# Kernel tuning notes

Hardware: AMD Instinct MI355X
Metric: run time of the kernel (lower is better)

## Reference

```python
import jax, jax.numpy as jnp
import numpy as np

H_MODEL = 1024
N_HEADS = 16
N_KV_HEADS = 4
HEAD_DIM = 64
SLIDING_WINDOW = 512
B, S = 2, 2048
NEG_INF = -1e9


def rotate_half(x):
    half = x.shape[-1] // 2
    return jnp.concatenate([-x[..., half:], x[..., :half]], axis=-1)


def setup_inputs() -> dict:
    key = jax.random.key(0)
    ks = jax.random.split(key, 8)
    hidden_states = jax.random.normal(ks[0], (B, S, H_MODEL), dtype=jnp.float32)
    # RoPE tables (HF style): cos/sin of shape [1, S, head_dim]
    inv_freq = 1.0 / (10000.0 ** (jnp.arange(0, HEAD_DIM, 2, dtype=jnp.float32) / HEAD_DIM))
    pos = jnp.arange(S, dtype=jnp.float32)
    freqs = jnp.einsum('s,d->sd', pos, inv_freq)            # [S, D/2]
    emb = jnp.concatenate([freqs, freqs], axis=-1)          # [S, D]
    cos = jnp.cos(emb)[None]                                # [1, S, D]
    sin = jnp.sin(emb)[None]
    # additive causal + sliding-window mask [1,1,S,S]
    i = jnp.arange(S)[:, None]
    j = jnp.arange(S)[None, :]
    allowed = (j <= i) & (i - j < SLIDING_WINDOW)
    attention_mask = jnp.where(allowed, 0.0, NEG_INF).astype(jnp.float32)[None, None]
    # projection weights (torch Linear stores [out, in]; y = x @ W.T)
    std = 0.02
    Wq = jax.random.normal(ks[1], (N_HEADS * HEAD_DIM, H_MODEL), dtype=jnp.float32) * std
    Wk = jax.random.normal(ks[2], (N_KV_HEADS * HEAD_DIM, H_MODEL), dtype=jnp.float32) * std
    Wv = jax.random.normal(ks[3], (N_KV_HEADS * HEAD_DIM, H_MODEL), dtype=jnp.float32) * std
    Wo = jax.random.normal(ks[4], (H_MODEL, N_HEADS * HEAD_DIM), dtype=jnp.float32) * std
    return {"hidden_states": hidden_states, "cos": cos, "sin": sin,
            "attention_mask": attention_mask, "Wq": Wq, "Wk": Wk, "Wv": Wv, "Wo": Wo}


def reference(hidden_states, cos, sin, attention_mask, Wq, Wk, Wv, Wo):
    b, s, _ = hidden_states.shape
    G = N_HEADS // N_KV_HEADS
    scaling = HEAD_DIM ** -0.5
    # QKV projections -> [B, H, S, D]
    q = jnp.einsum('bsh,oh->bso', hidden_states, Wq).reshape(b, s, N_HEADS, HEAD_DIM).transpose(0, 2, 1, 3)
    k = jnp.einsum('bsh,oh->bso', hidden_states, Wk).reshape(b, s, N_KV_HEADS, HEAD_DIM).transpose(0, 2, 1, 3)
    v = jnp.einsum('bsh,oh->bso', hidden_states, Wv).reshape(b, s, N_KV_HEADS, HEAD_DIM).transpose(0, 2, 1, 3)
    # RoPE (cos/sin broadcast over head dim via unsqueeze(1))
    c = cos[:, None, :, :]
    sn = sin[:, None, :, :]
    q = q * c + rotate_half(q) * sn
    k = k * c + rotate_half(k) * sn
    # GQA eager attention: group query heads over kv heads
    qg = q.reshape(b, N_KV_HEADS, G, s, HEAD_DIM)
    scores = jnp.einsum('bkgqd,bkpd->bkgqp', qg, k) * scaling  # [B,Hkv,G,S,S]
    scores = scores + attention_mask[:, :, None, :, :]
    probs = jax.nn.softmax(scores.astype(jnp.float32), axis=-1).astype(q.dtype)
    out = jnp.einsum('bkgqp,bkpd->bkgqd', probs, v)            # [B,Hkv,G,S,D]
    out = out.reshape(b, N_HEADS, s, HEAD_DIM).transpose(0, 2, 1, 3).reshape(b, s, N_HEADS * HEAD_DIM)
    return jnp.einsum('bso,ho->bsh', out, Wo)
```

## Files before the change

kernel.cpp:

```cpp
#include <hip/hip_runtime.h>
#include <hip/hip_bf16.h>

#define S_LEN 2048
#define NH 16
#define NKV 4
#define HD 64
#define WIN 512
#define BATCH 2

typedef __bf16 bf16_8 __attribute__((ext_vector_type(8)));
typedef float f32x4 __attribute__((ext_vector_type(4)));

__device__ inline bf16_8 cvt8(f32x4 a, f32x4 b) {
    bf16_8 r;
    r[0] = (__bf16)a[0]; r[1] = (__bf16)a[1]; r[2] = (__bf16)a[2]; r[3] = (__bf16)a[3];
    r[4] = (__bf16)b[0]; r[5] = (__bf16)b[1]; r[6] = (__bf16)b[2]; r[7] = (__bf16)b[3];
    return r;
}

typedef __attribute__((address_space(1))) const unsigned int guint;
typedef __attribute__((address_space(3))) unsigned int luint;
__device__ __forceinline__ void gload16(const void* g, void* l) {
    __builtin_amdgcn_global_load_lds((guint*)g, (luint*)l, 16, 0, 0);
}


__global__ __launch_bounds__(256) void cvt_pack(
    const float* __restrict__ hs, const float* __restrict__ Wq,
    const float* __restrict__ Wk, const float* __restrict__ Wv,
    const float* __restrict__ Wo,
    __bf16* __restrict__ hsp, __bf16* __restrict__ Wqp,
    __bf16* __restrict__ Wkp, __bf16* __restrict__ Wvp,
    __bf16* __restrict__ Wop)
{
    int i = blockIdx.x * 256 + threadIdx.x;
    const float* S; __bf16* P;
    if (i < 524288)      { S = hs; P = hsp; }
    else if (i < 655360) { S = Wq; P = Wqp; i -= 524288; }
    else if (i < 688128) { S = Wk; P = Wkp; i -= 655360; }
    else if (i < 720896) { S = Wv; P = Wvp; i -= 688128; }
    else                 { S = Wo; P = Wop; i -= 720896; }
    const int n = i >> 7;
    const int k = (i & 127) << 3;
    const f32x4 a = *(const f32x4*)(S + (size_t)n * 1024 + k);
    const f32x4 b = *(const f32x4*)(S + (size_t)n * 1024 + k + 4);
    const size_t dst = ((size_t)((n >> 4) * 32 + (k >> 5)) << 9)
                     + ((size_t)((n & 15) | (((k >> 3) & 3) << 4)) << 3);
    *(bf16_8*)(P + dst) = cvt8(a, b);
}

__device__ __forceinline__ void gemm64x128(
    const __bf16* __restrict__ Apk,
    const __bf16* __restrict__ Bp,
    int bx, int colb,
    __bf16* __restrict__ smem,
    int tid, f32x4 acc[2][4])
{
    const int wave = tid >> 6;
    const int lane = tid & 63;
    const int wm   = wave & 1;
    const int wn   = wave >> 1;
    const int lofs = lane << 3;
    const f32x4 fzero = {0.f, 0.f, 0.f, 0.f};
#pragma unroll
    for (int i = 0; i < 2; ++i)
#pragma unroll
        for (int nt = 0; nt < 4; ++nt) acc[i][nt] = fzero;

    __bf16* As = smem;
    __bf16* Bs = smem + 8192;

    const __bf16* aSrc  = Apk + ((size_t)(bx * 4 + wave) * 32) * 512 + lofs;
    const __bf16* bSrc0 = Bp + ((size_t)((colb >> 4) + wave * 2) * 32) * 512 + lofs;
    const __bf16* bSrc1 = Bp + ((size_t)((colb >> 4) + wave * 2 + 1) * 32) * 512 + lofs;

#define STAGE(buf, it) do {                                            \
        const int ko = (it) * 2;                                       \
        __bf16* ad = As + (buf) * 4096 + wave * 1024;                  \
        gload16(aSrc + (size_t)ko * 512,       ad);                    \
        gload16(aSrc + (size_t)(ko + 1) * 512, ad + 512);              \
        __bf16* bd = Bs + (buf) * 8192 + wave * 2048;                  \
        gload16(bSrc0 + (size_t)ko * 512,       bd);                   \
        gload16(bSrc0 + (size_t)(ko + 1) * 512, bd + 512);             \
        gload16(bSrc1 + (size_t)ko * 512,       bd + 1024);            \
        gload16(bSrc1 + (size_t)(ko + 1) * 512, bd + 1536);            \
    } while (0)

    STAGE(0, 0);
    __syncthreads();

#pragma unroll 2
    for (int it = 0; it < 16; ++it) {
        const int cur = it & 1;
        if (it < 15) STAGE(cur ^ 1, it + 1);

        const __bf16* Ab = As + cur * 4096;
        const __bf16* Bb = Bs + cur * 8192;
#pragma unroll
        for (int ks = 0; ks < 2; ++ks) {
            bf16_8 af[2], bf[4];
#pragma unroll
            for (int i = 0; i < 2; ++i)
                af[i] = *(const bf16_8*)(Ab + ((wm * 2 + i) * 2 + ks) * 512 + lofs);
#pragma unroll
            for (int nt = 0; nt < 4; ++nt)
                bf[nt] = *(const bf16_8*)(Bb + ((wn * 4 + nt) * 2 + ks) * 512 + lofs);
#pragma unroll
            for (int i = 0; i < 2; ++i)
#pragma unroll
                for (int nt = 0; nt < 4; ++nt)
                    acc[i][nt] = __builtin_amdgcn_mfma_f32_16x16x32_bf16(af[i], bf[nt], acc[i][nt], 0, 0, 0);
        }
        __syncthreads();
    }
#undef STAGE
}

__global__ __launch_bounds__(256) void gemm_qkv(
    const __bf16* __restrict__ Apk,
    const __bf16* __restrict__ Wqp,
    const __bf16* __restrict__ Wkp,
    const __bf16* __restrict__ Wvp,
    __bf16* __restrict__ Qp,
    __bf16* __restrict__ Kf,
    __bf16* __restrict__ Vf,
    const float* __restrict__ cosb,
    const float* __restrict__ sinb)
{
    __shared__ __align__(16) __bf16 smem[24576];

    const int tid  = threadIdx.x;
    const int wave = tid >> 6;
    const int lane = tid & 63;
    const int wm   = wave & 1;
    const int wn   = wave >> 1;
    const int fm   = lane & 15;

    const int bx   = blockIdx.x;
    const int row0 = bx * 64;
    const int by   = blockIdx.y;

    const __bf16* Bp; int colb; int mode;
    if (by < 8)       { Bp = Wqp; colb = by * 128;        mode = 0; }
    else if (by < 10) { Bp = Wkp; colb = (by - 8) * 128;  mode = 1; }
    else              { Bp = Wvp; colb = (by - 10) * 128; mode = 2; }
    const int col0 = colb;

    f32x4 acc[2][4];
    gemm64x128(Apk, Bp, bx, colb, smem, tid, acc);

    const int drow = (lane >> 4) << 2;
    const int cq   = col0 + wn * 64;
    const int bb   = row0 >> 11;
    const int sk0  = row0 & (S_LEN - 1);

    if (mode == 0) {
        const int lp = drow | ((fm >> 3) << 4);
#pragma unroll
        for (int i = 0; i < 2; ++i) {
            const size_t t1 = (size_t)(bx * 4 + wm * 2 + i) * 32 + (cq >> 5);
#pragma unroll
            for (int r = 0; r < 4; ++r) {
                const int row = row0 + wm * 32 + i * 16 + drow + r;
                const int s   = row & (S_LEN - 1);
#pragma unroll
                for (int nt = 0; nt < 2; ++nt) {
                    const int d = nt * 16 + fm;
                    const float c1 = cosb[s * HD + d];
                    const float s1 = sinb[s * HD + d];
                    const float c2 = cosb[s * HD + d + 32];
                    const float s2 = sinb[s * HD + d + 32];
                    const float x1 = acc[i][nt][r];
                    const float x2 = acc[i][nt + 2][r];
                    const size_t o = ((size_t)(lp + r + (nt * 2 << 4)) << 3) + (fm & 7);
                    Qp[(t1 << 9) + o]       = (__bf16)(x1 * c1 - x2 * s1);
                    Qp[((t1 + 1) << 9) + o] = (__bf16)(x2 * c2 + x1 * s2);
                }
            }
        }
    } else if (mode == 1) {
        __bf16* T = smem;
#pragma unroll
        for (int i = 0; i < 2; ++i) {
#pragma unroll
            for (int r = 0; r < 4; ++r) {
                const int kl = wm * 32 + i * 16 + drow + r;
                const int s  = sk0 + kl;
#pragma unroll
                for (int nt = 0; nt < 2; ++nt) {
                    const int d = nt * 16 + fm;
                    const float c1 = cosb[s * HD + d];
                    const float s1 = sinb[s * HD + d];
                    const float c2 = cosb[s * HD + d + 32];
                    const float s2 = sinb[s * HD + d + 32];
                    const float x1 = acc[i][nt][r];
                    const float x2 = acc[i][nt + 2][r];
                    T[kl * 136 + wn * 64 + d]      = (__bf16)(x1 * c1 - x2 * s1);
                    T[kl * 136 + wn * 64 + d + 32] = (__bf16)(x2 * c2 + x1 * s2);
                }
            }
        }
        __syncthreads();
#pragma unroll
        for (int c = 0; c < 4; ++c) {
            const int tile = c * 4 + wave;
            const int hh  = tile >> 3;
            const int kt4 = (tile >> 1) & 3;
            const int dd  = tile & 1;
            const int key = kt4 * 16 + fm;
            const int dl  = dd * 32 + ((lane >> 4) << 3);
            const bf16_8 v = *(const bf16_8*)&T[key * 136 + hh * 64 + dl];
            const int khg = (col0 + hh * 64) >> 6;
            const int ktg = (sk0 >> 4) + kt4;
            *(bf16_8*)&Kf[(size_t)(bb * NKV + khg) * 131072 + (size_t)(ktg * 2 + dd) * 512 + lane * 8] = v;
        }
    } else {
        __bf16* T2 = smem;
#pragma unroll
        for (int i = 0; i < 2; ++i)
#pragma unroll
            for (int r = 0; r < 4; ++r)
#pragma unroll
                for (int nt = 0; nt < 4; ++nt)
                    T2[(wn * 64 + nt * 16 + fm) * 72 + wm * 32 + i * 16 + drow + r] =
                        (__bf16)acc[i][nt][r];
        __syncthreads();
#pragma unroll
        for (int c = 0; c < 4; ++c) {
            const int tile = c * 4 + wave;
            const int hh  = tile >> 3;
            const int dd4 = (tile >> 1) & 3;
            const int ks  = tile & 1;
            const int dl  = dd4 * 16 + fm;
            const int key = ks * 32 + ((lane >> 4) << 3);
            const bf16_8 v = *(const bf16_8*)&T2[(hh * 64 + dl) * 72 + key];
            const int khg = (col0 + hh * 64) >> 6;
            const int kvg = (sk0 >> 5) + ks;
            *(bf16_8*)&Vf[(size_t)(bb * NKV + khg) * 131072 + (size_t)(dd4 * 64 + kvg) * 512 + lane * 8] = v;
        }
    }
}

__global__ __launch_bounds__(256) void gemm_o(
    const __bf16* __restrict__ Apk,
    const __bf16* __restrict__ Bp,
    float* __restrict__ C)
{
    __shared__ __align__(16) __bf16 smem[24576];

    const int tid  = threadIdx.x;
    const int wave = tid >> 6;
    const int lane = tid & 63;
    const int wm   = wave & 1;
    const int wn   = wave >> 1;

    const int bx   = blockIdx.x;
    const int row0 = bx * 64;
    const int colb = blockIdx.y * 128;

    f32x4 acc[2][4];
    gemm64x128(Apk, Bp, bx, colb, smem, tid, acc);

    const int fm = lane & 15;
    const int drow = (lane >> 4) << 2;
#pragma unroll
    for (int i = 0; i < 2; ++i)
#pragma unroll
        for (int r = 0; r < 4; ++r) {
            const int row = row0 + wm * 32 + i * 16 + drow + r;
#pragma unroll
            for (int nt = 0; nt < 4; ++nt)
                C[(size_t)row * 1024 + colb + wn * 64 + nt * 16 + fm] = acc[i][nt][r];
        }
}

__global__ __launch_bounds__(256) void attn_pk(const __bf16* __restrict__ Qp,
                                               const __bf16* __restrict__ Kf,
                                               const __bf16* __restrict__ Vf,
                                               __bf16* __restrict__ Op)
{
    __shared__ __align__(16) __bf16 Ps[4][16][72];

    const int tid  = threadIdx.x;
    const int wave = tid >> 6;
    const int lane = tid & 63;

    const int bid0 = blockIdx.x;
    const int bid  = (bid0 & 7) * 128 + (bid0 >> 3);

    const int qt = bid & (S_LEN / 64 - 1);
    const int h  = (bid >> 5) & (NH - 1);
    const int b  = bid >> 9;
    const int kh = h >> 2;

    const int q0 = qt * 64;
    const int qw = q0 + wave * 16;

    const int fm = lane & 15;

    const size_t qtile = ((size_t)((b * S_LEN + qw) >> 4) * 32 + h * 2) << 9;
    const bf16_8 qf0 = *(const bf16_8*)&Qp[qtile + (lane << 3)];
    const bf16_8 qf1 = *(const bf16_8*)&Qp[qtile + 512 + (lane << 3)];

    const __bf16* Kfb = Kf + (size_t)(b * NKV + kh) * 131072 + lane * 8;
    const __bf16* Vfb = Vf + (size_t)(b * NKV + kh) * 131072 + lane * 8;

    const f32x4 fzero = {0.f, 0.f, 0.f, 0.f};
    f32x4 oacc[4];
    float l[4];
#pragma unroll
    for (int nt = 0; nt < 4; ++nt) oacc[nt] = fzero;
#pragma unroll
    for (int r = 0; r < 4; ++r) l[r] = 0.f;

    const int qbase = qw + ((lane >> 4) << 2);
    const int fj = (lane >> 4) << 3;

    const int lo  = (qw >= WIN) ? ((qw - WIN + 1) & ~63) : 0;
    const int hi  = (qw + 15) & ~63;
    const int nit = ((hi - lo) >> 6) + 1;

    for (int it = 0; it < nit; ++it) {
        const int kb = lo + (it << 6);

        f32x4 sc[4];
        const int ktb = kb >> 4;
#pragma unroll
        for (int t4 = 0; t4 < 4; ++t4) {
            const bf16_8 k0 = *(const bf16_8*)(Kfb + (size_t)((ktb + t4) * 2) * 512);
            const bf16_8 k1 = *(const bf16_8*)(Kfb + (size_t)((ktb + t4) * 2 + 1) * 512);
            f32x4 s = fzero;
            s = __builtin_amdgcn_mfma_f32_16x16x32_bf16(qf0, k0, s, 0, 0, 0);
            s = __builtin_amdgcn_mfma_f32_16x16x32_bf16(qf1, k1, s, 0, 0, 0);
            sc[t4] = s;
        }

#pragma unroll
        for (int t4 = 0; t4 < 4; ++t4) {
            const int ki = kb + t4 * 16 + fm;
#pragma unroll
            for (int r = 0; r < 4; ++r) {
                const int qr = qbase + r;
                const float e = __expf(sc[t4][r] * 0.125f);
                const float p = (ki <= qr && qr - ki < WIN) ? e : 0.f;
                l[r] += p;
                Ps[wave][((lane >> 4) << 2) + r][t4 * 16 + fm] = (__bf16)p;
            }
        }

        const bf16_8 pf0 = *(const bf16_8*)&Ps[wave][fm][fj];
        const bf16_8 pf1 = *(const bf16_8*)&Ps[wave][fm][32 + fj];

        const int kvb = kb >> 5;
#pragma unroll
        for (int nt = 0; nt < 4; ++nt) {
            const bf16_8 v0 = *(const bf16_8*)(Vfb + (size_t)(nt * 64 + kvb) * 512);
            const bf16_8 v1 = *(const bf16_8*)(Vfb + (size_t)(nt * 64 + kvb + 1) * 512);
            oacc[nt] = __builtin_amdgcn_mfma_f32_16x16x32_bf16(pf0, v0, oacc[nt], 0, 0, 0);
            oacc[nt] = __builtin_amdgcn_mfma_f32_16x16x32_bf16(pf1, v1, oacc[nt], 0, 0, 0);
        }
    }

#pragma unroll
    for (int off = 8; off > 0; off >>= 1)
#pragma unroll
        for (int r = 0; r < 4; ++r)
            l[r] += __shfl_xor(l[r], off, 64);

    const int drow = (lane >> 4) << 2;
    float inv[4];
#pragma unroll
    for (int r = 0; r < 4; ++r) inv[r] = 1.0f / l[r];

    const size_t rt = (size_t)((b * S_LEN + qw) >> 4) * 32;
#pragma unroll
    for (int nt = 0; nt < 4; ++nt) {
        const size_t t = rt + h * 2 + (nt >> 1);
        const int lp0  = drow | (((nt * 2 + (fm >> 3)) & 3) << 4);
        const int e    = fm & 7;
#pragma unroll
        for (int r = 0; r < 4; ++r)
            Op[(t << 9) + ((size_t)(lp0 + r) << 3) + e] = (__bf16)(oacc[nt][r] * inv[r]);
    }
}

extern "C" void kernel_launch(void* const* d_in, const int* in_sizes, int n_in,
                              void* d_out, int out_size, void* d_ws, size_t ws_size,
                              hipStream_t stream)
{
    const float* hs   = (const float*)d_in[0];
    const float* cosb = (const float*)d_in[1];
    const float* sinb = (const float*)d_in[2];
    const float* Wq = (const float*)d_in[4];
    const float* Wk = (const float*)d_in[5];
    const float* Wv = (const float*)d_in[6];
    const float* Wo = (const float*)d_in[7];

    const int M = BATCH * S_LEN;

    __bf16* hsp = (__bf16*)d_ws;
    __bf16* Wqp = hsp + (size_t)M * 1024;
    __bf16* Wkp = Wqp + 1024 * 1024;
    __bf16* Wvp = Wkp + 256 * 1024;
    __bf16* Wop = Wvp + 256 * 1024;
    __bf16* Qpb = Wop + 1024 * 1024;
    __bf16* Kfb = Qpb + (size_t)M * 1024;
    __bf16* Vfb = Kfb + (size_t)8 * 131072;
    __bf16* Opb = Vfb + (size_t)8 * 131072;

    dim3 blk(256);
    cvt_pack<<<3328, blk, 0, stream>>>(hs, Wq, Wk, Wv, Wo,
                                       hsp, Wqp, Wkp, Wvp, Wop);

    gemm_qkv<<<dim3(64, 12), blk, 0, stream>>>(hsp, Wqp, Wkp, Wvp,
                                               Qpb, Kfb, Vfb, cosb, sinb);

    attn_pk<<<BATCH * NH * (S_LEN / 64), blk, 0, stream>>>(Qpb, Kfb, Vfb, Opb);

    gemm_o<<<dim3(64, 8), blk, 0, stream>>>(Opb, Wop, (float*)d_out);
}
```

Baseline: 157.0 us.

## Fuse all four stages into one cooperative persistent kernel with grid syncs

Merges the convert/pack, QKV GEMM with RoPE, attention, and output GEMM kernels into a single cooperative launch of 768 blocks, separated by grid-wide barriers. The aim is to remove the launch overhead and inter-kernel gaps of four separate launches. In exchange, attention runs with uneven work per block (1024 tiles spread over 768 blocks), the GEMM-O stage idles a third of the blocks, and the shared-memory footprint and register limits now come from the largest stage. If the cooperative launch fails, the code falls back to the original four launches.

```diff
diff --git a/kernel.cpp b/kernel.cpp
--- a/kernel.cpp
+++ b/kernel.cpp
@@ -1,5 +1,8 @@
 #include <hip/hip_runtime.h>
 #include <hip/hip_bf16.h>
+#include <hip/hip_cooperative_groups.h>
+
+namespace cg = cooperative_groups;
 
 #define S_LEN 2048
 #define NH 16
@@ -25,7 +28,7 @@
 }
 
 
-__global__ __launch_bounds__(256) void cvt_pack(
+__device__ __forceinline__ void cvt_body(int i,
     const float* __restrict__ hs, const float* __restrict__ Wq,
     const float* __restrict__ Wk, const float* __restrict__ Wv,
     const float* __restrict__ Wo,
@@ -33,7 +36,6 @@
     __bf16* __restrict__ Wkp, __bf16* __restrict__ Wvp,
     __bf16* __restrict__ Wop)
 {
-    int i = blockIdx.x * 256 + threadIdx.x;
     const float* S; __bf16* P;
     if (i < 524288)      { S = hs; P = hsp; }
     else if (i < 655360) { S = Wq; P = Wqp; i -= 524288; }
@@ -50,11 +52,8 @@
 }
 
 __device__ __forceinline__ void gemm64x128(
-    const __bf16* __restrict__ Apk,
-    const __bf16* __restrict__ Bp,
-    int bx, int colb,
-    __bf16* __restrict__ smem,
-    int tid, f32x4 acc[2][4])
+    const __bf16* __restrict__ Apk, const __bf16* __restrict__ Bp,
+    int bx, int colb, __bf16* __restrict__ smem, int tid, f32x4 acc[2][4])
 {
     const int wave = tid >> 6;
     const int lane = tid & 63;
@@ -116,29 +115,21 @@
 #undef STAGE
 }
 
-__global__ __launch_bounds__(256) void gemm_qkv(
+__device__ __forceinline__ void qkv_body(int bx, int by, int tid,
+    __bf16* __restrict__ smem,
     const __bf16* __restrict__ Apk,
-    const __bf16* __restrict__ Wqp,
-    const __bf16* __restrict__ Wkp,
+    const __bf16* __restrict__ Wqp, const __bf16* __restrict__ Wkp,
     const __bf16* __restrict__ Wvp,
-    __bf16* __restrict__ Qp,
-    __bf16* __restrict__ Kf,
-    __bf16* __restrict__ Vf,
-    const float* __restrict__ cosb,
-    const float* __restrict__ sinb)
-{
-    __shared__ __align__(16) __bf16 smem[24576];
-
-    const int tid  = threadIdx.x;
+    __bf16* __restrict__ Qp, __bf16* __restrict__ Kf, __bf16* __restrict__ Vf,
+    const float* __restrict__ cosb, const float* __restrict__ sinb)
+{
     const int wave = tid >> 6;
     const int lane = tid & 63;
     const int wm   = wave & 1;
     const int wn   = wave >> 1;
     const int fm   = lane & 15;
 
-    const int bx   = blockIdx.x;
     const int row0 = bx * 64;
-    const int by   = blockIdx.y;
 
     const __bf16* Bp; int colb; int mode;
     if (by < 8)       { Bp = Wqp; colb = by * 128;        mode = 0; }
@@ -241,51 +232,16 @@
     }
 }
 
-__global__ __launch_bounds__(256) void gemm_o(
-    const __bf16* __restrict__ Apk,
-    const __bf16* __restrict__ Bp,
-    float* __restrict__ C)
-{
-    __shared__ __align__(16) __bf16 smem[24576];
-
-    const int tid  = threadIdx.x;
+__device__ __forceinline__ void attn_body(int bid0, int tid,
+    __bf16* __restrict__ smem,
+    const __bf16* __restrict__ Qp, const __bf16* __restrict__ Kf,
+    const __bf16* __restrict__ Vf, __bf16* __restrict__ Op)
+{
+    __bf16 (*Ps)[16][72] = (__bf16(*)[16][72])smem;
+
     const int wave = tid >> 6;
     const int lane = tid & 63;
-    const int wm   = wave & 1;
-    const int wn   = wave >> 1;
-
-    const int bx   = blockIdx.x;
-    const int row0 = bx * 64;
-    const int colb = blockIdx.y * 128;
-
-    f32x4 acc[2][4];
-    gemm64x128(Apk, Bp, bx, colb, smem, tid, acc);
-
-    const int fm = lane & 15;
-    const int drow = (lane >> 4) << 2;
-#pragma unroll
-    for (int i = 0; i < 2; ++i)
-#pragma unroll
-        for (int r = 0; r < 4; ++r) {
-            const int row = row0 + wm * 32 + i * 16 + drow + r;
-#pragma unroll
-            for (int nt = 0; nt < 4; ++nt)
-                C[(size_t)row * 1024 + colb + wn * 64 + nt * 16 + fm] = acc[i][nt][r];
-        }
-}
-
-__global__ __launch_bounds__(256) void attn_pk(const __bf16* __restrict__ Qp,
-                                               const __bf16* __restrict__ Kf,
-                                               const __bf16* __restrict__ Vf,
-                                               __bf16* __restrict__ Op)
-{
-    __shared__ __align__(16) __bf16 Ps[4][16][72];
-
-    const int tid  = threadIdx.x;
-    const int wave = tid >> 6;
-    const int lane = tid & 63;
-
-    const int bid0 = blockIdx.x;
+
     const int bid  = (bid0 & 7) * 128 + (bid0 >> 3);
 
     const int qt = bid & (S_LEN / 64 - 1);
@@ -382,6 +338,111 @@
         for (int r = 0; r < 4; ++r)
             Op[(t << 9) + ((size_t)(lp0 + r) << 3) + e] = (__bf16)(oacc[nt][r] * inv[r]);
     }
+}
+
+__device__ __forceinline__ void gemmo_body(int bx, int by, int tid,
+    __bf16* __restrict__ smem,
+    const __bf16* __restrict__ Apk, const __bf16* __restrict__ Bp,
+    float* __restrict__ C)
+{
+    const int wave = tid >> 6;
+    const int lane = tid & 63;
+    const int wm   = wave & 1;
+    const int wn   = wave >> 1;
+
+    const int row0 = bx * 64;
+    const int colb = by * 128;
+
+    f32x4 acc[2][4];
+    gemm64x128(Apk, Bp, bx, colb, smem, tid, acc);
+
+    const int fm = lane & 15;
+    const int drow = (lane >> 4) << 2;
+#pragma unroll
+    for (int i = 0; i < 2; ++i)
+#pragma unroll
+        for (int r = 0; r < 4; ++r) {
+            const int row = row0 + wm * 32 + i * 16 + drow + r;
+#pragma unroll
+            for (int nt = 0; nt < 4; ++nt)
+                C[(size_t)row * 1024 + colb + wn * 64 + nt * 16 + fm] = acc[i][nt][r];
+        }
+}
+
+__global__ __launch_bounds__(256, 3) void fused(
+    const float* __restrict__ hs, const float* __restrict__ cosb,
+    const float* __restrict__ sinb,
+    const float* __restrict__ Wq, const float* __restrict__ Wk,
+    const float* __restrict__ Wv, const float* __restrict__ Wo,
+    __bf16* __restrict__ hsp, __bf16* __restrict__ Wqp,
+    __bf16* __restrict__ Wkp, __bf16* __restrict__ Wvp,
+    __bf16* __restrict__ Wop,
+    __bf16* __restrict__ Qp, __bf16* __restrict__ Kf,
+    __bf16* __restrict__ Vf, __bf16* __restrict__ Op,
+    float* __restrict__ C)
+{
+    __shared__ __align__(16) __bf16 smem[24576];
+    cg::grid_group grid = cg::this_grid();
+
+    const int blk = blockIdx.x;
+    const int tid = threadIdx.x;
+
+    for (int i = blk * 256 + tid; i < 851968; i += 768 * 256)
+        cvt_body(i, hs, Wq, Wk, Wv, Wo, hsp, Wqp, Wkp, Wvp, Wop);
+
+    grid.sync();
+
+    qkv_body(blk & 63, blk >> 6, tid, smem, hsp, Wqp, Wkp, Wvp,
+             Qp, Kf, Vf, cosb, sinb);
+
+    grid.sync();
+
+    for (int v = blk; v < 1024; v += 768)
+        attn_body(v, tid, smem, Qp, Kf, Vf, Op);
+
+    grid.sync();
+
+    if (blk < 512)
+        gemmo_body(blk & 63, blk >> 6, tid, smem, Op, Wop, C);
+}
+
+__global__ __launch_bounds__(256) void cvt_pack(
+    const float* __restrict__ hs, const float* __restrict__ Wq,
+    const float* __restrict__ Wk, const float* __restrict__ Wv,
+    const float* __restrict__ Wo,
+    __bf16* __restrict__ hsp, __bf16* __restrict__ Wqp,
+    __bf16* __restrict__ Wkp, __bf16* __restrict__ Wvp,
+    __bf16* __restrict__ Wop)
+{
+    cvt_body(blockIdx.x * 256 + threadIdx.x, hs, Wq, Wk, Wv, Wo,
+             hsp, Wqp, Wkp, Wvp, Wop);
+}
+
+__global__ __launch_bounds__(256) void gemm_qkv(
+    const __bf16* __restrict__ Apk, const __bf16* __restrict__ Wqp,
+    const __bf16* __restrict__ Wkp, const __bf16* __restrict__ Wvp,
+    __bf16* __restrict__ Qp, __bf16* __restrict__ Kf, __bf16* __restrict__ Vf,
+    const float* __restrict__ cosb, const float* __restrict__ sinb)
+{
+    __shared__ __align__(16) __bf16 smem[24576];
+    qkv_body(blockIdx.x, blockIdx.y, threadIdx.x, smem, Apk, Wqp, Wkp, Wvp,
+             Qp, Kf, Vf, cosb, sinb);
+}
+
+__global__ __launch_bounds__(256) void attn_pk(
+    const __bf16* __restrict__ Qp, const __bf16* __restrict__ Kf,
+    const __bf16* __restrict__ Vf, __bf16* __restrict__ Op)
+{
+    __shared__ __align__(16) __bf16 smem[4608];
+    attn_body(blockIdx.x, threadIdx.x, smem, Qp, Kf, Vf, Op);
+}
+
+__global__ __launch_bounds__(256) void gemm_o(
+    const __bf16* __restrict__ Apk, const __bf16* __restrict__ Bp,
+    float* __restrict__ C)
+{
+    __shared__ __align__(16) __bf16 smem[24576];
+    gemmo_body(blockIdx.x, blockIdx.y, threadIdx.x, smem, Apk, Bp, C);
 }
 
 extern "C" void kernel_launch(void* const* d_in, const int* in_sizes, int n_in,
@@ -407,15 +468,25 @@
     __bf16* Kfb = Qpb + (size_t)M * 1024;
     __bf16* Vfb = Kfb + (size_t)8 * 131072;
     __bf16* Opb = Vfb + (size_t)8 * 131072;
-
-    dim3 blk(256);
-    cvt_pack<<<3328, blk, 0, stream>>>(hs, Wq, Wk, Wv, Wo,
-                                       hsp, Wqp, Wkp, Wvp, Wop);
-
-    gemm_qkv<<<dim3(64, 12), blk, 0, stream>>>(hsp, Wqp, Wkp, Wvp,
-                                               Qpb, Kfb, Vfb, cosb, sinb);
-
-    attn_pk<<<BATCH * NH * (S_LEN / 64), blk, 0, stream>>>(Qpb, Kfb, Vfb, Opb);
-
-    gemm_o<<<dim3(64, 8), blk, 0, stream>>>(Opb, Wop, (float*)d_out);
-}
+    float*  Cp  = (float*)d_out;
+
+    void* kargs[] = {
+        (void*)&hs,  (void*)&cosb, (void*)&sinb,
+        (void*)&Wq,  (void*)&Wk,   (void*)&Wv,  (void*)&Wo,
+        (void*)&hsp, (void*)&Wqp,  (void*)&Wkp, (void*)&Wvp, (void*)&Wop,
+        (void*)&Qpb, (void*)&Kfb,  (void*)&Vfb, (void*)&Opb, (void*)&Cp
+    };
+
+    hipError_t e = hipLaunchCooperativeKernel(
+        (const void*)fused, dim3(768), dim3(256), kargs, 0, stream);
+
+    if (e != hipSuccess) {
+        dim3 blk(256);
+        cvt_pack<<<3328, blk, 0, stream>>>(hs, Wq, Wk, Wv, Wo,
+                                           hsp, Wqp, Wkp, Wvp, Wop);
+        gemm_qkv<<<dim3(64, 12), blk, 0, stream>>>(hsp, Wqp, Wkp, Wvp,
+                                                   Qpb, Kfb, Vfb, cosb, sinb);
+        attn_pk<<<BATCH * NH * (S_LEN / 64), blk, 0, stream>>>(Qpb, Kfb, Vfb, Opb);
+        gemm_o<<<dim3(64, 8), blk, 0, stream>>>(Opb, Wop, Cp);
+    }
+}
```

After: 489.8 us. 3.12x slower.

## Fuse fp32-to-bf16 conversion into GEMM loaders and drop cvt_pack kernel

Applied to the files above, without the earlier changes.

Removes the separate conversion and packing kernel. The QKV and output-projection GEMMs now read fp32 activations and weights straight from global memory into registers, convert them to bf16 and write them into the packed LDS layout, with register prefetch of the next k-tile overlapping the MFMA work. This saves one launch and a full round trip of bf16 copies through global memory. In exchange each GEMM block re-reads and re-converts fp32 data, so global traffic per block is doubled and more registers are needed. Launch bounds now request 3 blocks per SM.

```diff
diff --git a/kernel.cpp b/kernel.cpp
--- a/kernel.cpp
+++ b/kernel.cpp
@@ -25,42 +25,20 @@
 }
 
 
-__global__ __launch_bounds__(256) void cvt_pack(
-    const float* __restrict__ hs, const float* __restrict__ Wq,
-    const float* __restrict__ Wk, const float* __restrict__ Wv,
-    const float* __restrict__ Wo,
-    __bf16* __restrict__ hsp, __bf16* __restrict__ Wqp,
-    __bf16* __restrict__ Wkp, __bf16* __restrict__ Wvp,
-    __bf16* __restrict__ Wop)
-{
-    int i = blockIdx.x * 256 + threadIdx.x;
-    const float* S; __bf16* P;
-    if (i < 524288)      { S = hs; P = hsp; }
-    else if (i < 655360) { S = Wq; P = Wqp; i -= 524288; }
-    else if (i < 688128) { S = Wk; P = Wkp; i -= 655360; }
-    else if (i < 720896) { S = Wv; P = Wvp; i -= 688128; }
-    else                 { S = Wo; P = Wop; i -= 720896; }
-    const int n = i >> 7;
-    const int k = (i & 127) << 3;
-    const f32x4 a = *(const f32x4*)(S + (size_t)n * 1024 + k);
-    const f32x4 b = *(const f32x4*)(S + (size_t)n * 1024 + k + 4);
-    const size_t dst = ((size_t)((n >> 4) * 32 + (k >> 5)) << 9)
-                     + ((size_t)((n & 15) | (((k >> 3) & 3) << 4)) << 3);
-    *(bf16_8*)(P + dst) = cvt8(a, b);
-}
-
-__device__ __forceinline__ void gemm64x128(
-    const __bf16* __restrict__ Apk,
-    const __bf16* __restrict__ Bp,
-    int bx, int colb,
-    __bf16* __restrict__ smem,
-    int tid, f32x4 acc[2][4])
+__device__ __forceinline__ void gemm64x128_f32(
+    const float* __restrict__ A32,
+    const float* __restrict__ B32,
+    int row0, int colb,
+    __bf16* __restrict__ smem, int tid, f32x4 acc[2][4])
 {
     const int wave = tid >> 6;
     const int lane = tid & 63;
     const int wm   = wave & 1;
     const int wn   = wave >> 1;
     const int lofs = lane << 3;
+    const int sr   = lane >> 2;
+    const int sc   = (lane & 3) << 3;
+    const int pl8  = ((sr) | ((lane & 3) << 4)) << 3;
     const f32x4 fzero = {0.f, 0.f, 0.f, 0.f};
 #pragma unroll
     for (int i = 0; i < 2; ++i)
@@ -70,29 +48,39 @@
     __bf16* As = smem;
     __bf16* Bs = smem + 8192;
 
-    const __bf16* aSrc  = Apk + ((size_t)(bx * 4 + wave) * 32) * 512 + lofs;
-    const __bf16* bSrc0 = Bp + ((size_t)((colb >> 4) + wave * 2) * 32) * 512 + lofs;
-    const __bf16* bSrc1 = Bp + ((size_t)((colb >> 4) + wave * 2 + 1) * 32) * 512 + lofs;
-
-#define STAGE(buf, it) do {                                            \
-        const int ko = (it) * 2;                                       \
-        __bf16* ad = As + (buf) * 4096 + wave * 1024;                  \
-        gload16(aSrc + (size_t)ko * 512,       ad);                    \
-        gload16(aSrc + (size_t)(ko + 1) * 512, ad + 512);              \
-        __bf16* bd = Bs + (buf) * 8192 + wave * 2048;                  \
-        gload16(bSrc0 + (size_t)ko * 512,       bd);                   \
-        gload16(bSrc0 + (size_t)(ko + 1) * 512, bd + 512);             \
-        gload16(bSrc1 + (size_t)ko * 512,       bd + 1024);            \
-        gload16(bSrc1 + (size_t)(ko + 1) * 512, bd + 1536);            \
-    } while (0)
-
-    STAGE(0, 0);
+    const float* aS = A32 + (size_t)(row0 + wave * 16 + sr) * 1024 + sc;
+    const float* bS = B32 + (size_t)(colb + wave * 32 + sr) * 1024 + sc;
+
+    f32x4 ra[2][2], rb[2][2][2];
+
+#define LOADS(it) do { const int ko = (it) * 64;                               \
+        _Pragma("unroll") for (int ks = 0; ks < 2; ++ks) {                     \
+            ra[ks][0] = *(const f32x4*)(aS + ko + ks * 32);                    \
+            ra[ks][1] = *(const f32x4*)(aS + ko + ks * 32 + 4);                \
+            _Pragma("unroll") for (int gg = 0; gg < 2; ++gg) {                 \
+                rb[gg][ks][0] = *(const f32x4*)(bS + gg * 16384 + ko + ks * 32);     \
+                rb[gg][ks][1] = *(const f32x4*)(bS + gg * 16384 + ko + ks * 32 + 4); \
+            }                                                                  \
+        } } while (0)
+
+#define WRITES(buf) do {                                                       \
+        _Pragma("unroll") for (int ks = 0; ks < 2; ++ks) {                     \
+            *(bf16_8*)(As + (buf) * 4096 + (wave * 2 + ks) * 512 + pl8) =      \
+                cvt8(ra[ks][0], ra[ks][1]);                                    \
+            _Pragma("unroll") for (int gg = 0; gg < 2; ++gg)                   \
+                *(bf16_8*)(Bs + (buf) * 8192 + ((wave * 2 + gg) * 2 + ks) * 512 + pl8) = \
+                    cvt8(rb[gg][ks][0], rb[gg][ks][1]);                        \
+        } } while (0)
+
+    LOADS(0);
+    WRITES(0);
     __syncthreads();
 
 #pragma unroll 2
     for (int it = 0; it < 16; ++it) {
         const int cur = it & 1;
-        if (it < 15) STAGE(cur ^ 1, it + 1);
+        const bool pf = it < 15;
+        if (pf) LOADS(it + 1);
 
         const __bf16* Ab = As + cur * 4096;
         const __bf16* Bb = Bs + cur * 8192;
@@ -111,21 +99,107 @@
                 for (int nt = 0; nt < 4; ++nt)
                     acc[i][nt] = __builtin_amdgcn_mfma_f32_16x16x32_bf16(af[i], bf[nt], acc[i][nt], 0, 0, 0);
         }
+
+        if (pf) WRITES(cur ^ 1);
         __syncthreads();
     }
-#undef STAGE
-}
-
-__global__ __launch_bounds__(256) void gemm_qkv(
-    const __bf16* __restrict__ Apk,
-    const __bf16* __restrict__ Wqp,
-    const __bf16* __restrict__ Wkp,
-    const __bf16* __restrict__ Wvp,
+#undef LOADS
+#undef WRITES
+}
+
+__device__ __forceinline__ void gemm64x128_mix(
+    const __bf16* __restrict__ Apk, const float* __restrict__ B32,
+    int bx, int colb, __bf16* __restrict__ smem, int tid, f32x4 acc[2][4])
+{
+    const int wave = tid >> 6;
+    const int lane = tid & 63;
+    const int wm   = wave & 1;
+    const int wn   = wave >> 1;
+    const int lofs = lane << 3;
+    const int sr   = lane >> 2;
+    const int sc   = (lane & 3) << 3;
+    const int pl8  = ((sr) | ((lane & 3) << 4)) << 3;
+    const f32x4 fzero = {0.f, 0.f, 0.f, 0.f};
+#pragma unroll
+    for (int i = 0; i < 2; ++i)
+#pragma unroll
+        for (int nt = 0; nt < 4; ++nt) acc[i][nt] = fzero;
+
+    __bf16* As = smem;
+    __bf16* Bs = smem + 8192;
+
+    const __bf16* aSrc = Apk + ((size_t)(bx * 4 + wave) * 32) * 512 + lofs;
+    const float*  bS   = B32 + (size_t)(colb + wave * 32 + sr) * 1024 + sc;
+
+    f32x4 rb[2][2][2];
+
+#define STAGEA(buf, it) do { const int ko = (it) * 2;                          \
+        __bf16* ad = As + (buf) * 4096 + wave * 1024;                          \
+        gload16(aSrc + (size_t)ko * 512,       ad);                            \
+        gload16(aSrc + (size_t)(ko + 1) * 512, ad + 512);                      \
+    } while (0)
+
+#define LOADSB(it) do { const int ko = (it) * 64;                              \
+        _Pragma("unroll") for (int ks = 0; ks < 2; ++ks)                       \
+            _Pragma("unroll") for (int gg = 0; gg < 2; ++gg) {                 \
+                rb[gg][ks][0] = *(const f32x4*)(bS + gg * 16384 + ko + ks * 32);     \
+                rb[gg][ks][1] = *(const f32x4*)(bS + gg * 16384 + ko + ks * 32 + 4); \
+            } } while (0)
+
+#define WRITESB(buf) do {                                                      \
+        _Pragma("unroll") for (int ks = 0; ks < 2; ++ks)                       \
+            _Pragma("unroll") for (int gg = 0; gg < 2; ++gg)                   \
+                *(bf16_8*)(Bs + (buf) * 8192 + ((wave * 2 + gg) * 2 + ks) * 512 + pl8) = \
+                    cvt8(rb[gg][ks][0], rb[gg][ks][1]);                        \
+        } while (0)
+
+    STAGEA(0, 0);
+    LOADSB(0);
+    WRITESB(0);
+    __syncthreads();
+
+#pragma unroll 2
+    for (int it = 0; it < 16; ++it) {
+        const int cur = it & 1;
+        const bool pf = it < 15;
+        if (pf) {
+            STAGEA(cur ^ 1, it + 1);
+            LOADSB(it + 1);
+        }
+
+        const __bf16* Ab = As + cur * 4096;
+        const __bf16* Bb = Bs + cur * 8192;
+#pragma unroll
+        for (int ks = 0; ks < 2; ++ks) {
+            bf16_8 af[2], bf[4];
+#pragma unroll
+            for (int i = 0; i < 2; ++i)
+                af[i] = *(const bf16_8*)(Ab + ((wm * 2 + i) * 2 + ks) * 512 + lofs);
+#pragma unroll
+            for (int nt = 0; nt < 4; ++nt)
+                bf[nt] = *(const bf16_8*)(Bb + ((wn * 4 + nt) * 2 + ks) * 512 + lofs);
+#pragma unroll
+            for (int i = 0; i < 2; ++i)
+#pragma unroll
+                for (int nt = 0; nt < 4; ++nt)
+                    acc[i][nt] = __builtin_amdgcn_mfma_f32_16x16x32_bf16(af[i], bf[nt], acc[i][nt], 0, 0, 0);
+        }
+
+        if (pf) WRITESB(cur ^ 1);
+        __syncthreads();
+    }
+#undef STAGEA
+#undef LOADSB
+#undef WRITESB
+}
+
+__global__ __launch_bounds__(256, 3) void gemm_qkv(
+    const float* __restrict__ hs,
+    const float* __restrict__ Wq, const float* __restrict__ Wk,
+    const float* __restrict__ Wv,
     __bf16* __restrict__ Qp,
-    __bf16* __restrict__ Kf,
-    __bf16* __restrict__ Vf,
-    const float* __restrict__ cosb,
-    const float* __restrict__ sinb)
+    __bf16* __restrict__ Kf, __bf16* __restrict__ Vf,
+    const float* __restrict__ cosb, const float* __restrict__ sinb)
 {
     __shared__ __align__(16) __bf16 smem[24576];
 
@@ -140,14 +214,14 @@
     const int row0 = bx * 64;
     const int by   = blockIdx.y;
 
-    const __bf16* Bp; int colb; int mode;
-    if (by < 8)       { Bp = Wqp; colb = by * 128;        mode = 0; }
-    else if (by < 10) { Bp = Wkp; colb = (by - 8) * 128;  mode = 1; }
-    else              { Bp = Wvp; colb = (by - 10) * 128; mode = 2; }
+    const float* Bp; int colb; int mode;
+    if (by < 8)       { Bp = Wq; colb = by * 128;        mode = 0; }
+    else if (by < 10) { Bp = Wk; colb = (by - 8) * 128;  mode = 1; }
+    else              { Bp = Wv; colb = (by - 10) * 128; mode = 2; }
     const int col0 = colb;
 
     f32x4 acc[2][4];
-    gemm64x128(Apk, Bp, bx, colb, smem, tid, acc);
+    gemm64x128_f32(hs, Bp, row0, colb, smem, tid, acc);
 
     const int drow = (lane >> 4) << 2;
     const int cq   = col0 + wn * 64;
@@ -241,9 +315,9 @@
     }
 }
 
-__global__ __launch_bounds__(256) void gemm_o(
+__global__ __launch_bounds__(256, 3) void gemm_o(
     const __bf16* __restrict__ Apk,
-    const __bf16* __restrict__ Bp,
+    const float* __restrict__ Wo,
     float* __restrict__ C)
 {
     __shared__ __align__(16) __bf16 smem[24576];
@@ -259,7 +333,7 @@
     const int colb = blockIdx.y * 128;
 
     f32x4 acc[2][4];
-    gemm64x128(Apk, Bp, bx, colb, smem, tid, acc);
+    gemm64x128_mix(Apk, Wo, bx, colb, smem, tid, acc);
 
     const int fm = lane & 15;
     const int drow = (lane >> 4) << 2;
@@ -398,24 +472,16 @@
 
     const int M = BATCH * S_LEN;
 
-    __bf16* hsp = (__bf16*)d_ws;
-    __bf16* Wqp = hsp + (size_t)M * 1024;
-    __bf16* Wkp = Wqp + 1024 * 1024;
-    __bf16* Wvp = Wkp + 256 * 1024;
-    __bf16* Wop = Wvp + 256 * 1024;
-    __bf16* Qpb = Wop + 1024 * 1024;
+    __bf16* Qpb = (__bf16*)d_ws;
     __bf16* Kfb = Qpb + (size_t)M * 1024;
     __bf16* Vfb = Kfb + (size_t)8 * 131072;
     __bf16* Opb = Vfb + (size_t)8 * 131072;
 
     dim3 blk(256);
-    cvt_pack<<<3328, blk, 0, stream>>>(hs, Wq, Wk, Wv, Wo,
-                                       hsp, Wqp, Wkp, Wvp, Wop);
-
-    gemm_qkv<<<dim3(64, 12), blk, 0, stream>>>(hsp, Wqp, Wkp, Wvp,
+    gemm_qkv<<<dim3(64, 12), blk, 0, stream>>>(hs, Wq, Wk, Wv,
                                                Qpb, Kfb, Vfb, cosb, sinb);
 
     attn_pk<<<BATCH * NH * (S_LEN / 64), blk, 0, stream>>>(Qpb, Kfb, Vfb, Opb);
 
-    gemm_o<<<dim3(64, 8), blk, 0, stream>>>(Opb, Wop, (float*)d_out);
-}
+    gemm_o<<<dim3(64, 8), blk, 0, stream>>>(Opb, Wo, (float*)d_out);
+}
```

Measured after the change: 167.7 us. 1.07x slower.

## Triple-buffer GEMM LDS staging with explicit vmcnt waits and raw barriers

Applied to the files above, without the earlier changes.

Replaces the double-buffered async global-to-LDS pipeline in the shared 64x128 GEMM helper with a three-stage ring. Loads run two iterations ahead, and explicit s_waitcnt vmcnt counts stand in for full __syncthreads, so more memory latency is hidden behind MFMA work. Shared memory per block grows from 48KB to 72KB, which can lower occupancy. Extra syncs were added before the K/V epilogues because they reuse the staging buffer.

```diff
diff --git a/kernel.cpp b/kernel.cpp
--- a/kernel.cpp
+++ b/kernel.cpp
@@ -67,35 +67,36 @@
 #pragma unroll
         for (int nt = 0; nt < 4; ++nt) acc[i][nt] = fzero;
 
-    __bf16* As = smem;
-    __bf16* Bs = smem + 8192;
-
     const __bf16* aSrc  = Apk + ((size_t)(bx * 4 + wave) * 32) * 512 + lofs;
     const __bf16* bSrc0 = Bp + ((size_t)((colb >> 4) + wave * 2) * 32) * 512 + lofs;
     const __bf16* bSrc1 = Bp + ((size_t)((colb >> 4) + wave * 2 + 1) * 32) * 512 + lofs;
 
 #define STAGE(buf, it) do {                                            \
-        const int ko = (it) * 2;                                       \
-        __bf16* ad = As + (buf) * 4096 + wave * 1024;                  \
-        gload16(aSrc + (size_t)ko * 512,       ad);                    \
-        gload16(aSrc + (size_t)(ko + 1) * 512, ad + 512);              \
-        __bf16* bd = Bs + (buf) * 8192 + wave * 2048;                  \
-        gload16(bSrc0 + (size_t)ko * 512,       bd);                   \
-        gload16(bSrc0 + (size_t)(ko + 1) * 512, bd + 512);             \
-        gload16(bSrc1 + (size_t)ko * 512,       bd + 1024);            \
-        gload16(bSrc1 + (size_t)(ko + 1) * 512, bd + 1536);            \
+        __bf16* base = smem + (buf) * 12288;                           \
+        gload16(aSrc + (size_t)(it) * 1024,       base + wave * 1024); \
+        gload16(aSrc + (size_t)(it) * 1024 + 512, base + wave * 1024 + 512); \
+        __bf16* bd = base + 4096 + wave * 2048;                        \
+        gload16(bSrc0 + (size_t)(it) * 1024,       bd);                \
+        gload16(bSrc0 + (size_t)(it) * 1024 + 512, bd + 512);          \
+        gload16(bSrc1 + (size_t)(it) * 1024,       bd + 1024);         \
+        gload16(bSrc1 + (size_t)(it) * 1024 + 512, bd + 1536);         \
     } while (0)
 
     STAGE(0, 0);
-    __syncthreads();
-
-#pragma unroll 2
+    STAGE(1, 1);
+
+#pragma unroll
     for (int it = 0; it < 16; ++it) {
-        const int cur = it & 1;
-        if (it < 15) STAGE(cur ^ 1, it + 1);
-
-        const __bf16* Ab = As + cur * 4096;
-        const __bf16* Bb = Bs + cur * 8192;
+        if (it < 14) STAGE((it + 2) % 3, it + 2);
+
+        if (it < 14)       asm volatile("s_waitcnt vmcnt(12)" ::: "memory");
+        else if (it == 14) asm volatile("s_waitcnt vmcnt(6)"  ::: "memory");
+        else               asm volatile("s_waitcnt vmcnt(0)"  ::: "memory");
+        __builtin_amdgcn_sched_barrier(0);
+        __builtin_amdgcn_s_barrier();
+
+        const __bf16* Ab = smem + (it % 3) * 12288;
+        const __bf16* Bb = Ab + 4096;
 #pragma unroll
         for (int ks = 0; ks < 2; ++ks) {
             bf16_8 af[2], bf[4];
@@ -111,7 +112,7 @@
                 for (int nt = 0; nt < 4; ++nt)
                     acc[i][nt] = __builtin_amdgcn_mfma_f32_16x16x32_bf16(af[i], bf[nt], acc[i][nt], 0, 0, 0);
         }
-        __syncthreads();
+        __builtin_amdgcn_s_barrier();
     }
 #undef STAGE
 }
@@ -127,7 +128,7 @@
     const float* __restrict__ cosb,
     const float* __restrict__ sinb)
 {
-    __shared__ __align__(16) __bf16 smem[24576];
+    __shared__ __align__(16) __bf16 smem[36864];
 
     const int tid  = threadIdx.x;
     const int wave = tid >> 6;
@@ -180,6 +181,7 @@
         }
     } else if (mode == 1) {
         __bf16* T = smem;
+        __syncthreads();
 #pragma unroll
         for (int i = 0; i < 2; ++i) {
 #pragma unroll
@@ -216,6 +218,7 @@
         }
     } else {
         __bf16* T2 = smem;
+        __syncthreads();
 #pragma unroll
         for (int i = 0; i < 2; ++i)
 #pragma unroll
@@ -246,7 +249,7 @@
     const __bf16* __restrict__ Bp,
     float* __restrict__ C)
 {
-    __shared__ __align__(16) __bf16 smem[24576];
+    __shared__ __align__(16) __bf16 smem[36864];
 
     const int tid  = threadIdx.x;
     const int wave = tid >> 6;
```

After: 154.5 us (median of 2 runs). About the same (-1.6%).
